# Kernel optimization log

Hardware: AMD Instinct MI355X
Metric: run time of the kernel (lower is better)

Reference implementation:

```python
import jax, jax.numpy as jnp
import numpy as np

WS = 8        # window size
NH = 8        # num heads


def setup_inputs() -> dict:
    key = jax.random.key(0)
    ks = jax.random.split(key, 6)
    B, C, H, W = 8, 256, 64, 64
    Cr = C // 4
    s = lambda n: 1.0 / np.sqrt(n)
    return {
        "x": jax.random.normal(ks[0], (B, C, H, W), jnp.float32),
        "ca_w1": jax.random.normal(ks[1], (Cr, C), jnp.float32) * s(C),
        "ca_b1": jnp.zeros((Cr,), jnp.float32),
        "ca_w2": jax.random.normal(ks[2], (C, Cr), jnp.float32) * s(Cr),
        "ca_b2": jnp.zeros((C,), jnp.float32),
        "in_proj_w": jax.random.normal(ks[3], (3 * C, C), jnp.float32) * s(C),
        "in_proj_b": jnp.zeros((3 * C,), jnp.float32),
        "out_proj_w": jax.random.normal(ks[4], (C, C), jnp.float32) * s(C),
        "out_proj_b": jnp.zeros((C,), jnp.float32),
    }


def reference(x, ca_w1, ca_b1, ca_w2, ca_b2, in_proj_w, in_proj_b, out_proj_w, out_proj_b):
    B, C, H, W = x.shape
    # ---- channel SE gate: AdaptiveAvgPool2d(1) -> 1x1 conv == linear ----
    pooled = x.mean(axis=(2, 3))                                   # [B, C]
    h1 = jax.nn.relu(pooled @ ca_w1.T + ca_b1)                     # [B, C/4]
    ca = jax.nn.sigmoid(h1 @ ca_w2.T + ca_b2)                      # [B, C]
    x = x * ca[:, :, None, None]

    # ---- window partition (non-overlapping unfold) ----
    Hw, Ww = H // WS, W // WS
    nwin = Hw * Ww
    xw = x.reshape(B, C, Hw, WS, Ww, WS).transpose(0, 1, 2, 4, 3, 5)   # [B,C,Hw,Ww,ws,ws]
    # view(B,C,nwin,ws*ws).permute(2,0,3,1).reshape(nwin*B, ws*ws, C)
    xw = xw.reshape(B, C, nwin, WS * WS).transpose(2, 0, 3, 1).reshape(nwin * B, WS * WS, C)

    # ---- nn.MultiheadAttention with batch_first=False: (L, N, E) ----
    # L = nwin*B (sequence!), N = ws*ws (batch!), E = C  -- faithful to source quirk
    L, N, _ = xw.shape
    hd = C // NH
    qkv = xw @ in_proj_w.T + in_proj_b                             # [L, N, 3C]
    q, k, v = jnp.split(qkv, 3, axis=-1)
    to_heads = lambda t: t.reshape(L, N, NH, hd).transpose(1, 2, 0, 3)  # [N, NH, L, hd]
    q, k, v = to_heads(q), to_heads(k), to_heads(v)
    scale = 1.0 / jnp.sqrt(jnp.asarray(hd, x.dtype))
    attn = jax.nn.softmax(jnp.einsum("nhld,nhmd->nhlm", q * scale, k), axis=-1)
    o = jnp.einsum("nhlm,nhmd->nhld", attn, v)                     # [N, NH, L, hd]
    o = o.transpose(2, 0, 1, 3).reshape(L, N, C)
    o = o @ out_proj_w.T + out_proj_b                              # [L, N, C]

    # ---- reshape back; nearest interpolate H*W -> H*W is identity ----
    o = o.reshape(nwin, B, WS * WS, C).transpose(1, 3, 0, 2)       # [B, C, nwin, ws*ws]
    x_out = o.reshape(B, C, H, W)
    return x + x_out
```

## Files before the change

### kernel.cpp

```cpp
#include <hip/hip_runtime.h>
#include <hip/hip_bf16.h>
#include <math.h>


typedef unsigned short ushort_t;
typedef unsigned int uint_t;
typedef __attribute__((ext_vector_type(8))) short bf16x8;
typedef __attribute__((ext_vector_type(4))) float f32x4;

#define ALPHA 0.25503486f

__device__ __forceinline__ uint_t pk_rne(float a, float b) {
    __hip_bfloat16 ha = __float2bfloat16(a), hb = __float2bfloat16(b);
    ushort_t ua = *(ushort_t*)&ha, ub = *(ushort_t*)&hb;
    return (uint_t)ua | ((uint_t)ub << 16);
}

__device__ __forceinline__ uint_t pk2(float a, float b) {
    union { float f; uint_t u; } ua, ub; ua.f = a; ub.f = b;
    return __builtin_amdgcn_perm(ua.u, ub.u, 0x03020706u);
}

__device__ __forceinline__ void gl_lds16(const ushort_t* g, ushort_t* l) {
    __builtin_amdgcn_global_load_lds(
        (__attribute__((address_space(1))) unsigned int*)(g),
        (__attribute__((address_space(3))) unsigned int*)(l), 16, 0, 0);
}

__global__ __launch_bounds__(256) void k_pool(const float* __restrict__ x,
                                              float* __restrict__ pooled) {
    int bc = blockIdx.x;
    const float4* row4 = (const float4*)(x + (size_t)bc * 4096);
    float s = 0.f;
    for (int i = threadIdx.x; i < 1024; i += 256) {
        float4 v = row4[i];
        s += v.x + v.y + v.z + v.w;
    }
    __shared__ float red[256];
    red[threadIdx.x] = s;
    __syncthreads();
    for (int o = 128; o > 0; o >>= 1) {
        if (threadIdx.x < o) red[threadIdx.x] += red[threadIdx.x + o];
        __syncthreads();
    }
    if (threadIdx.x == 0) pooled[bc] = red[0] * (1.f / 4096.f);
}

__global__ __launch_bounds__(256) void k_se(const float* __restrict__ pooled,
                                            const float* __restrict__ w1,
                                            const float* __restrict__ b1,
                                            const float* __restrict__ w2,
                                            const float* __restrict__ b2,
                                            float* __restrict__ ca) {
    __shared__ float sp[2048];
    __shared__ float sh1[512];
    int t = threadIdx.x;
    for (int i = t; i < 2048; i += 256) sp[i] = pooled[i];
    __syncthreads();
    for (int o = t; o < 512; o += 256) {
        int b = o >> 6, m = o & 63;
        float s = b1[m];
        const float* wr = w1 + (size_t)m * 256;
        const float* pr = sp + b * 256;
        for (int c = 0; c < 256; c++) s += pr[c] * wr[c];
        sh1[o] = s > 0.f ? s : 0.f;
    }
    __syncthreads();
    for (int o = t; o < 2048; o += 256) {
        int b = o >> 8, m = o & 255;
        float s = b2[m];
        const float* wr = w2 + (size_t)m * 64;
        const float* hr = sh1 + b * 64;
        for (int c = 0; c < 64; c++) s += hr[c] * wr[c];
        ca[o] = 1.f / (1.f + __expf(-s));
    }
}

__global__ __launch_bounds__(256) void k_cvt(const float* __restrict__ src,
                                             ushort_t* __restrict__ dst, int n8,
                                             int scale_n8, float scale) {
    int i = blockIdx.x * 256 + threadIdx.x;
    if (i >= n8) return;
    float sc = (i < scale_n8) ? scale : 1.f;
    const float4* s = (const float4*)src + (size_t)i * 2;
    float4 a = s[0], b = s[1];
    uint4 u;
    u.x = pk_rne(a.x * sc, a.y * sc); u.y = pk_rne(a.z * sc, a.w * sc);
    u.z = pk_rne(b.x * sc, b.y * sc); u.w = pk_rne(b.z * sc, b.w * sc);
    *(uint4*)(dst + (size_t)i * 8) = u;
}

#define GPAD 524
__global__ __launch_bounds__(256) void k_gate(const float* __restrict__ x,
                                              const float* __restrict__ ca,
                                              ushort_t* __restrict__ Ab) {
    __shared__ __align__(16) ushort_t Ls[32 * GPAD];
    __shared__ float sca[32];
    int bx = blockIdx.x;
    int b = bx >> 6, hw = (bx >> 3) & 7, c0 = (bx & 7) * 32;
    int t = threadIdx.x;
    if (t < 32) sca[t] = ca[b * 256 + c0 + t];
    __syncthreads();
    const float4* xb = (const float4*)(x + ((size_t)(b * 256 + c0) * 64 + hw * 8) * 64);
#pragma unroll
    for (int i = 0; i < 16; i++) {
        int f = i * 256 + t;
        int ch = f >> 7, rem = f & 127, r = rem >> 4, w4 = rem & 15;
        float4 v = xb[(size_t)ch * 1024 + r * 16 + w4];
        float g = sca[ch];
        uint2 u;
        u.x = pk_rne(v.x * g, v.y * g);
        u.y = pk_rne(v.z * g, v.w * g);
        *(uint2*)&Ls[ch * GPAD + r * 64 + w4 * 4] = u;
    }
    __syncthreads();
#pragma unroll
    for (int i = 0; i < 8; i++) {
        int q = i * 256 + t;
        int rr = q >> 2, part = q & 3;
        int ww = rr >> 6, p = rr & 63;
        int px = (p >> 3) * 64 + ww * 8 + (p & 7);
        const ushort_t* ls = &Ls[part * 8 * GPAD + px];
        uint4 u;
        u.x = (uint_t)ls[0]        | ((uint_t)ls[GPAD] << 16);
        u.y = (uint_t)ls[2 * GPAD] | ((uint_t)ls[3 * GPAD] << 16);
        u.z = (uint_t)ls[4 * GPAD] | ((uint_t)ls[5 * GPAD] << 16);
        u.w = (uint_t)ls[6 * GPAD] | ((uint_t)ls[7 * GPAD] << 16);
        size_t m = (size_t)(((hw * 8 + ww) * 8 + b) * 64 + p);
        *(uint4*)(Ab + m * 256 + c0 + part * 8) = u;
    }
}

__global__ __launch_bounds__(256, 2) void k_gemm_qkv2(const ushort_t* __restrict__ A,
                                                      const ushort_t* __restrict__ Bw,
                                                      const float* __restrict__ bias,
                                                      ushort_t* __restrict__ Qb,
                                                      ushort_t* __restrict__ Kb,
                                                      ushort_t* __restrict__ Vb) {
    __shared__ __align__(16) ushort_t As[2][8192];
    __shared__ __align__(16) ushort_t Bs[2][8192];
    int tid = threadIdx.x;
    int lane = tid & 63, wave = tid >> 6;
    int wm = wave >> 1, wn = wave & 1;
    int col = lane & 15, quad = lane >> 4;
    int orig = blockIdx.x;
    int wgid = (orig & 7) * 192 + (orig >> 3);
    int n0 = (wgid % 6) * 128;
    int m0 = (wgid / 6) * 128;
    int cbase = wave * 64 + lane;

    const ushort_t* asrc[4];
    const ushort_t* bsrc[4];
#pragma unroll
    for (int q = 0; q < 4; q++) {
        int c = q * 256 + cbase;
        int row = c >> 3;
        int kp = (c & 7) ^ (row & 7);
        asrc[q] = A + (size_t)(m0 + row) * 256 + kp * 8;
        bsrc[q] = Bw + (size_t)(n0 + row) * 256 + kp * 8;
    }

    f32x4 acc[4][4];
#pragma unroll
    for (int i = 0; i < 4; i++)
#pragma unroll
        for (int j = 0; j < 4; j++) acc[i][j] = (f32x4){0.f, 0.f, 0.f, 0.f};

#pragma unroll
    for (int q = 0; q < 4; q++) {
        gl_lds16(asrc[q], &As[0][(q * 4 + wave) * 512]);
        gl_lds16(bsrc[q], &Bs[0][(q * 4 + wave) * 512]);
    }
    __syncthreads();

#pragma unroll
    for (int t = 0; t < 4; t++) {
        if (t < 3) {
            int k0 = (t + 1) * 64;
            int nb = (t + 1) & 1;
#pragma unroll
            for (int q = 0; q < 4; q++) {
                gl_lds16(asrc[q] + k0, &As[nb][(q * 4 + wave) * 512]);
                gl_lds16(bsrc[q] + k0, &Bs[nb][(q * 4 + wave) * 512]);
            }
        }
        const ushort_t* Ac = As[t & 1];
        const ushort_t* Bc = Bs[t & 1];
#pragma unroll
        for (int kk = 0; kk < 2; kk++) {
            bf16x8 af[4], bfg[4];
#pragma unroll
            for (int i = 0; i < 4; i++) {
                int row = wm * 64 + i * 16 + col;
                af[i] = *(const bf16x8*)&Ac[row * 64 + ((kk * 4 + quad) ^ (row & 7)) * 8];
            }
#pragma unroll
            for (int j = 0; j < 4; j++) {
                int row = wn * 64 + j * 16 + col;
                bfg[j] = *(const bf16x8*)&Bc[row * 64 + ((kk * 4 + quad) ^ (row & 7)) * 8];
            }
#pragma unroll
            for (int i = 0; i < 4; i++)
#pragma unroll
                for (int j = 0; j < 4; j++)
                    acc[i][j] = __builtin_amdgcn_mfma_f32_16x16x32_bf16(bfg[j], af[i], acc[i][j], 0, 0, 0);
        }
        __syncthreads();
    }

    int sec = n0 >> 8;
    ushort_t* dst = (sec == 0) ? Qb : (sec == 1) ? Kb : Vb;
    float bsc = (sec == 0) ? ALPHA : 1.f;
    int nb = (n0 & 255) + wn * 64 + quad * 4;
#pragma unroll
    for (int j = 0; j < 4; j++) {
        float4 bv = *(const float4*)(bias + n0 + wn * 64 + j * 16 + quad * 4);
        bv.x *= bsc; bv.y *= bsc; bv.z *= bsc; bv.w *= bsc;
#pragma unroll
        for (int i = 0; i < 4; i++) {
            int m = m0 + wm * 64 + i * 16 + col;
            uint2 st;
            st.x = pk_rne(acc[i][j][0] + bv.x, acc[i][j][1] + bv.y);
            st.y = pk_rne(acc[i][j][2] + bv.z, acc[i][j][3] + bv.w);
            *(uint2*)(dst + (size_t)m * 256 + nb + j * 16) = st;
        }
    }
}

__global__ __launch_bounds__(512, 4) void k_attn(const ushort_t* __restrict__ Qb,
                                                 const ushort_t* __restrict__ Kb,
                                                 const ushort_t* __restrict__ Vb,
                                                 ushort_t* __restrict__ AO) {
    __shared__ __align__(16) ushort_t Ks[512 * 32];
    __shared__ __align__(16) ushort_t Vt[32 * 512];
    int p = blockIdx.x >> 3, h = blockIdx.x & 7;
    int tid = threadIdx.x;
    int lane = tid & 63, wave = tid >> 6;
    int col = lane & 15, quad = lane >> 4;

#pragma unroll
    for (int it = 0; it < 4; it++) {
        int u = it * 512 + tid;
        int key = u >> 2, oct = u & 3;
        size_t grow = ((size_t)(key * 64 + p)) * 256 + h * 32 + oct * 8;
        int ck = oct ^ ((key >> 3) & 3);
        *(bf16x8*)&Ks[key * 32 + ck * 8] = *(const bf16x8*)(Kb + grow);
    }
#pragma unroll
    for (int it = 0; it < 2; it++) {
        int u = it * 512 + tid;
        int kp = u >> 2, oct = u & 3;
        int k0 = kp * 2;
        size_t g0 = ((size_t)(k0 * 64 + p)) * 256 + h * 32 + oct * 8;
        bf16x8 v0 = *(const bf16x8*)(Vb + g0);
        bf16x8 v1 = *(const bf16x8*)(Vb + g0 + 16384);
        int kc = kp >> 2;
#pragma unroll
        for (int j = 0; j < 8; j++) {
            int vc = oct * 8 + j;
            int kcs = kc ^ (vc & 7) ^ ((vc >> 3) << 1);
            uint_t pkv = (uint_t)(ushort_t)v0[j] | ((uint_t)(ushort_t)v1[j] << 16);
            *(uint_t*)&Vt[vc * 512 + kcs * 8 + (k0 & 7)] = pkv;
        }
    }

    bf16x8 qfrag[4];
#pragma unroll
    for (int i = 0; i < 4; i++) {
        int qt = wave * 4 + i;
        qfrag[i] = *(const bf16x8*)(Qb + ((size_t)((qt * 16 + col) * 64 + p)) * 256 + h * 32 + quad * 8);
    }

    f32x4 O0[4], O1[4];
    float qsum[4];
#pragma unroll
    for (int i = 0; i < 4; i++) {
        O0[i] = (f32x4){0.f, 0.f, 0.f, 0.f};
        O1[i] = (f32x4){0.f, 0.f, 0.f, 0.f};
        qsum[i] = 0.f;
    }
    const f32x4 zero = {0.f, 0.f, 0.f, 0.f};
    int R = col >> 2, r4 = lane & 3;
    int krow0 = 8 * R + r4;
    int vc0 = col, vc1 = col + 16;
    int sw0 = (vc0 & 7) ^ ((vc0 >> 3) << 1);
    int sw1 = (vc1 & 7) ^ ((vc1 >> 3) << 1);

    __syncthreads();

    for (int c = 0; c < 512; c += 32) {
        int row0 = c + krow0;
        int row1 = row0 + 4;
        int ckq = quad ^ ((row0 >> 3) & 3);
        bf16x8 kf0 = *(const bf16x8*)&Ks[row0 * 32 + ckq * 8];
        bf16x8 kf1 = *(const bf16x8*)&Ks[row1 * 32 + ckq * 8];
        int kc = (c >> 3) + quad;
        bf16x8 vf0 = *(const bf16x8*)&Vt[vc0 * 512 + ((kc ^ sw0) * 8)];
        bf16x8 vf1 = *(const bf16x8*)&Vt[vc1 * 512 + ((kc ^ sw1) * 8)];
#pragma unroll
        for (int i = 0; i < 4; i++) {
            f32x4 s0 = __builtin_amdgcn_mfma_f32_16x16x32_bf16(kf0, qfrag[i], zero, 0, 0, 0);
            f32x4 s1 = __builtin_amdgcn_mfma_f32_16x16x32_bf16(kf1, qfrag[i], zero, 0, 0, 0);
            float p0[4], p1[4];
#pragma unroll
            for (int r = 0; r < 4; r++) {
                p0[r] = __builtin_amdgcn_exp2f(s0[r]);
                p1[r] = __builtin_amdgcn_exp2f(s1[r]);
            }
            qsum[i] += ((p0[0] + p0[1]) + (p0[2] + p0[3])) + ((p1[0] + p1[1]) + (p1[2] + p1[3]));
            union { uint_t u[4]; bf16x8 v; } pb;
            pb.u[0] = pk2(p0[0], p0[1]);
            pb.u[1] = pk2(p0[2], p0[3]);
            pb.u[2] = pk2(p1[0], p1[1]);
            pb.u[3] = pk2(p1[2], p1[3]);
            O0[i] = __builtin_amdgcn_mfma_f32_16x16x32_bf16(vf0, pb.v, O0[i], 0, 0, 0);
            O1[i] = __builtin_amdgcn_mfma_f32_16x16x32_bf16(vf1, pb.v, O1[i], 0, 0, 0);
        }
    }

#pragma unroll
    for (int i = 0; i < 4; i++) {
        float s = qsum[i];
        s += __shfl_xor(s, 16);
        s += __shfl_xor(s, 32);
        float inv = 1.f / s;
        int qt = wave * 4 + i;
        ushort_t* dst = AO + ((size_t)((qt * 16 + col) * 64 + p)) * 256 + h * 32;
        uint2 st0, st1;
        st0.x = pk_rne(O0[i][0] * inv, O0[i][1] * inv);
        st0.y = pk_rne(O0[i][2] * inv, O0[i][3] * inv);
        st1.x = pk_rne(O1[i][0] * inv, O1[i][1] * inv);
        st1.y = pk_rne(O1[i][2] * inv, O1[i][3] * inv);
        *(uint2*)(dst + quad * 4) = st0;
        *(uint2*)(dst + 16 + quad * 4) = st1;
    }
}

__global__ __launch_bounds__(256, 2) void k_gemm_out2(const ushort_t* __restrict__ A,
                                                      const ushort_t* __restrict__ Bw,
                                                      const float* __restrict__ bias,
                                                      const float* __restrict__ x,
                                                      const float* __restrict__ ca,
                                                      float* __restrict__ out) {
    __shared__ __align__(16) ushort_t As[2][8192];
    __shared__ __align__(16) ushort_t Bs[2][8192];
    int tid = threadIdx.x;
    int lane = tid & 63, wave = tid >> 6;
    int wm = wave >> 1, wn = wave & 1;
    int col = lane & 15, quad = lane >> 4;
    int orig = blockIdx.x;
    int wgid = (orig & 7) * 64 + (orig >> 3);
    int n0 = (wgid & 1) * 128;
    int m0 = (wgid >> 1) * 128;
    int cbase = wave * 64 + lane;

    const ushort_t* asrc[4];
    const ushort_t* bsrc[4];
#pragma unroll
    for (int q = 0; q < 4; q++) {
        int c = q * 256 + cbase;
        int row = c >> 3;
        int kp = (c & 7) ^ (row & 7);
        asrc[q] = A + (size_t)(m0 + row) * 256 + kp * 8;
        bsrc[q] = Bw + (size_t)(n0 + row) * 256 + kp * 8;
    }

    f32x4 acc[4][4];
#pragma unroll
    for (int i = 0; i < 4; i++)
#pragma unroll
        for (int j = 0; j < 4; j++) acc[i][j] = (f32x4){0.f, 0.f, 0.f, 0.f};

#pragma unroll
    for (int q = 0; q < 4; q++) {
        gl_lds16(asrc[q], &As[0][(q * 4 + wave) * 512]);
        gl_lds16(bsrc[q], &Bs[0][(q * 4 + wave) * 512]);
    }
    __syncthreads();

#pragma unroll
    for (int t = 0; t < 4; t++) {
        if (t < 3) {
            int k0 = (t + 1) * 64;
            int nb = (t + 1) & 1;
#pragma unroll
            for (int q = 0; q < 4; q++) {
                gl_lds16(asrc[q] + k0, &As[nb][(q * 4 + wave) * 512]);
                gl_lds16(bsrc[q] + k0, &Bs[nb][(q * 4 + wave) * 512]);
            }
        }
        const ushort_t* Ac = As[t & 1];
        const ushort_t* Bc = Bs[t & 1];
#pragma unroll
        for (int kk = 0; kk < 2; kk++) {
            bf16x8 af[4], bfg[4];
#pragma unroll
            for (int i = 0; i < 4; i++) {
                int row = wm * 64 + i * 16 + col;
                af[i] = *(const bf16x8*)&Ac[row * 64 + ((kk * 4 + quad) ^ (row & 7)) * 8];
            }
#pragma unroll
            for (int j = 0; j < 4; j++) {
                int row = wn * 64 + j * 16 + col;
                bfg[j] = *(const bf16x8*)&Bc[row * 64 + ((kk * 4 + quad) ^ (row & 7)) * 8];
            }
#pragma unroll
            for (int i = 0; i < 4; i++)
#pragma unroll
                for (int j = 0; j < 4; j++)
                    acc[i][j] = __builtin_amdgcn_mfma_f32_16x16x32_bf16(bfg[j], af[i], acc[i][j], 0, 0, 0);
        }
        __syncthreads();
    }

    int lw = (m0 + wm * 64) >> 6;
    int b = lw & 7, w_idx = lw >> 3;
#pragma unroll
    for (int j = 0; j < 4; j++) {
        int nbase = n0 + wn * 64 + j * 16 + quad * 4;
        float4 bv = *(const float4*)(bias + nbase);
        float4 cv = *(const float4*)(ca + b * 256 + nbase);
#pragma unroll
        for (int i = 0; i < 4; i++) {
            int p = i * 16 + col;
#pragma unroll
            for (int r = 0; r < 4; r++) {
                int n = nbase + r;
                float bias_r = (r == 0) ? bv.x : (r == 1) ? bv.y : (r == 2) ? bv.z : bv.w;
                float ca_r = (r == 0) ? cv.x : (r == 1) ? cv.y : (r == 2) ? cv.z : cv.w;
                size_t oi = (((size_t)b * 256 + n) * 64 + w_idx) * 64 + p;
                out[oi] = acc[i][j][r] + bias_r + x[oi] * ca_r;
            }
        }
    }
}

extern "C" void kernel_launch(void* const* d_in, const int* in_sizes, int n_in,
                              void* d_out, int out_size, void* d_ws, size_t ws_size,
                              hipStream_t stream) {
    const float* x     = (const float*)d_in[0];
    const float* ca_w1 = (const float*)d_in[1];
    const float* ca_b1 = (const float*)d_in[2];
    const float* ca_w2 = (const float*)d_in[3];
    const float* ca_b2 = (const float*)d_in[4];
    const float* ipw   = (const float*)d_in[5];
    const float* ipb   = (const float*)d_in[6];
    const float* opw   = (const float*)d_in[7];
    const float* opb   = (const float*)d_in[8];
    float* out = (float*)d_out;

    char* ws = (char*)d_ws;
    const size_t MB16 = 16777216ull;
    ushort_t* Qb = (ushort_t*)(ws + 0);
    ushort_t* Kb = (ushort_t*)(ws + MB16);
    ushort_t* Vb = (ushort_t*)(ws + 2 * MB16);
    float* pooled = (float*)(ws + 3 * MB16);
    float* ca     = (float*)(ws + 3 * MB16 + 8192);

    ushort_t* Ab  = (ushort_t*)d_out;
    ushort_t* Wqb = (ushort_t*)((char*)d_out + MB16);
    ushort_t* Wob = Vb;

    k_cvt<<<96, 256, 0, stream>>>(ipw, Wqb, 24576, 8192, ALPHA);
    k_pool<<<2048, 256, 0, stream>>>(x, pooled);
    k_se<<<1, 256, 0, stream>>>(pooled, ca_w1, ca_b1, ca_w2, ca_b2, ca);
    k_gate<<<512, 256, 0, stream>>>(x, ca, Ab);
    k_gemm_qkv2<<<1536, 256, 0, stream>>>(Ab, Wqb, ipb, Qb, Kb, Vb);
    k_attn<<<512, 512, 0, stream>>>(Qb, Kb, Vb, Qb );
    k_cvt<<<32, 256, 0, stream>>>(opw, Wob, 8192, 0, 1.f);
    k_gemm_out2<<<512, 256, 0, stream>>>(Qb, Wob, opb, x, ca, out);
}
```

Measured before the change: 208.5 us.

## Fuse pooling with weight conversion and widen QKV GEMM tile to 128x256

Pooling and both weight bf16 conversions now run in one launch. When the workspace is large enough, the out-proj conversion moves early into a dedicated workspace slot, removing one later launch. The QKV GEMM now computes a 128x256 tile (a full Q, K or V section) per block with half the blocks, which raises B-tile reuse. It drops LDS double buffering for a single buffer loaded each k-step, so load latency may no longer be hidden, and it uses more accumulator registers.

```diff
diff --git a/kernel.cpp b/kernel.cpp
--- a/kernel.cpp
+++ b/kernel.cpp
@@ -27,52 +27,46 @@
         (__attribute__((address_space(3))) unsigned int*)(l), 16, 0, 0);
 }
 
-__global__ __launch_bounds__(256) void k_pool(const float* __restrict__ x,
-                                              float* __restrict__ pooled) {
-    int bc = blockIdx.x;
-    const float4* row4 = (const float4*)(x + (size_t)bc * 4096);
-    float s = 0.f;
-    for (int i = threadIdx.x; i < 1024; i += 256) {
-        float4 v = row4[i];
-        s += v.x + v.y + v.z + v.w;
-    }
-    __shared__ float red[256];
-    red[threadIdx.x] = s;
-    __syncthreads();
-    for (int o = 128; o > 0; o >>= 1) {
-        if (threadIdx.x < o) red[threadIdx.x] += red[threadIdx.x + o];
+__global__ __launch_bounds__(256) void k_pre(const float* __restrict__ x,
+                                             float* __restrict__ pooled,
+                                             const float* __restrict__ ipw,
+                                             ushort_t* __restrict__ Wqb,
+                                             const float* __restrict__ opw,
+                                             ushort_t* __restrict__ Wob) {
+    int bx = blockIdx.x;
+    int t = threadIdx.x;
+    if (bx < 2048) {
+        const float4* row4 = (const float4*)(x + (size_t)bx * 4096);
+        float s = 0.f;
+        for (int i = t; i < 1024; i += 256) {
+            float4 v = row4[i];
+            s += v.x + v.y + v.z + v.w;
+        }
+        __shared__ float red[256];
+        red[t] = s;
         __syncthreads();
-    }
-    if (threadIdx.x == 0) pooled[bc] = red[0] * (1.f / 4096.f);
-}
-
-__global__ __launch_bounds__(256) void k_se(const float* __restrict__ pooled,
-                                            const float* __restrict__ w1,
-                                            const float* __restrict__ b1,
-                                            const float* __restrict__ w2,
-                                            const float* __restrict__ b2,
-                                            float* __restrict__ ca) {
-    __shared__ float sp[2048];
-    __shared__ float sh1[512];
-    int t = threadIdx.x;
-    for (int i = t; i < 2048; i += 256) sp[i] = pooled[i];
-    __syncthreads();
-    for (int o = t; o < 512; o += 256) {
-        int b = o >> 6, m = o & 63;
-        float s = b1[m];
-        const float* wr = w1 + (size_t)m * 256;
-        const float* pr = sp + b * 256;
-        for (int c = 0; c < 256; c++) s += pr[c] * wr[c];
-        sh1[o] = s > 0.f ? s : 0.f;
-    }
-    __syncthreads();
-    for (int o = t; o < 2048; o += 256) {
-        int b = o >> 8, m = o & 255;
-        float s = b2[m];
-        const float* wr = w2 + (size_t)m * 64;
-        const float* hr = sh1 + b * 64;
-        for (int c = 0; c < 64; c++) s += hr[c] * wr[c];
-        ca[o] = 1.f / (1.f + __expf(-s));
+        for (int o = 128; o > 0; o >>= 1) {
+            if (t < o) red[t] += red[t + o];
+            __syncthreads();
+        }
+        if (t == 0) pooled[bx] = red[0] * (1.f / 4096.f);
+    } else if (bx < 2144) {
+        int i = (bx - 2048) * 256 + t;
+        float sc = (i < 8192) ? ALPHA : 1.f;
+        const float4* s4 = (const float4*)ipw + (size_t)i * 2;
+        float4 a = s4[0], b = s4[1];
+        uint4 u;
+        u.x = pk_rne(a.x * sc, a.y * sc); u.y = pk_rne(a.z * sc, a.w * sc);
+        u.z = pk_rne(b.x * sc, b.y * sc); u.w = pk_rne(b.z * sc, b.w * sc);
+        *(uint4*)(Wqb + (size_t)i * 8) = u;
+    } else {
+        int i = (bx - 2144) * 256 + t;
+        const float4* s4 = (const float4*)opw + (size_t)i * 2;
+        float4 a = s4[0], b = s4[1];
+        uint4 u;
+        u.x = pk_rne(a.x, a.y); u.y = pk_rne(a.z, a.w);
+        u.z = pk_rne(b.x, b.y); u.w = pk_rne(b.z, b.w);
+        *(uint4*)(Wob + (size_t)i * 8) = u;
     }
 }
 
@@ -88,6 +82,36 @@
     u.x = pk_rne(a.x * sc, a.y * sc); u.y = pk_rne(a.z * sc, a.w * sc);
     u.z = pk_rne(b.x * sc, b.y * sc); u.w = pk_rne(b.z * sc, b.w * sc);
     *(uint4*)(dst + (size_t)i * 8) = u;
+}
+
+__global__ __launch_bounds__(256) void k_se(const float* __restrict__ pooled,
+                                            const float* __restrict__ w1,
+                                            const float* __restrict__ b1,
+                                            const float* __restrict__ w2,
+                                            const float* __restrict__ b2,
+                                            float* __restrict__ ca) {
+    __shared__ float sp[2048];
+    __shared__ float sh1[512];
+    int t = threadIdx.x;
+    for (int i = t; i < 2048; i += 256) sp[i] = pooled[i];
+    __syncthreads();
+    for (int o = t; o < 512; o += 256) {
+        int b = o >> 6, m = o & 63;
+        float s = b1[m];
+        const float* wr = w1 + (size_t)m * 256;
+        const float* pr = sp + b * 256;
+        for (int c = 0; c < 256; c++) s += pr[c] * wr[c];
+        sh1[o] = s > 0.f ? s : 0.f;
+    }
+    __syncthreads();
+    for (int o = t; o < 2048; o += 256) {
+        int b = o >> 8, m = o & 255;
+        float s = b2[m];
+        const float* wr = w2 + (size_t)m * 64;
+        const float* hr = sh1 + b * 64;
+        for (int c = 0; c < 64; c++) s += hr[c] * wr[c];
+        ca[o] = 1.f / (1.f + __expf(-s));
+    }
 }
 
 #define GPAD 524
@@ -131,90 +155,85 @@
     }
 }
 
-__global__ __launch_bounds__(256, 2) void k_gemm_qkv2(const ushort_t* __restrict__ A,
+__global__ __launch_bounds__(256, 2) void k_gemm_qkv3(const ushort_t* __restrict__ A,
                                                       const ushort_t* __restrict__ Bw,
                                                       const float* __restrict__ bias,
                                                       ushort_t* __restrict__ Qb,
                                                       ushort_t* __restrict__ Kb,
                                                       ushort_t* __restrict__ Vb) {
-    __shared__ __align__(16) ushort_t As[2][8192];
-    __shared__ __align__(16) ushort_t Bs[2][8192];
+    __shared__ __align__(16) ushort_t As[8192];
+    __shared__ __align__(16) ushort_t Bs[16384];
     int tid = threadIdx.x;
     int lane = tid & 63, wave = tid >> 6;
     int wm = wave >> 1, wn = wave & 1;
     int col = lane & 15, quad = lane >> 4;
     int orig = blockIdx.x;
-    int wgid = (orig & 7) * 192 + (orig >> 3);
-    int n0 = (wgid % 6) * 128;
-    int m0 = (wgid / 6) * 128;
+    int xcd = orig & 7;
+    int i96 = orig >> 3;
+    int mi = i96 / 3;
+    int sec = i96 - mi * 3;
+    int m0 = (xcd * 32 + mi) * 128;
+    const ushort_t* Bsec = Bw + ((size_t)sec << 16);
+
     int cbase = wave * 64 + lane;
-
     const ushort_t* asrc[4];
-    const ushort_t* bsrc[4];
+    const ushort_t* bsrc[8];
 #pragma unroll
     for (int q = 0; q < 4; q++) {
         int c = q * 256 + cbase;
         int row = c >> 3;
         int kp = (c & 7) ^ (row & 7);
         asrc[q] = A + (size_t)(m0 + row) * 256 + kp * 8;
-        bsrc[q] = Bw + (size_t)(n0 + row) * 256 + kp * 8;
-    }
-
-    f32x4 acc[4][4];
+    }
+#pragma unroll
+    for (int q = 0; q < 8; q++) {
+        int c = q * 256 + cbase;
+        int row = c >> 3;
+        int kp = (c & 7) ^ (row & 7);
+        bsrc[q] = Bsec + (size_t)row * 256 + kp * 8;
+    }
+
+    f32x4 acc[4][8];
 #pragma unroll
     for (int i = 0; i < 4; i++)
 #pragma unroll
-        for (int j = 0; j < 4; j++) acc[i][j] = (f32x4){0.f, 0.f, 0.f, 0.f};
-
-#pragma unroll
-    for (int q = 0; q < 4; q++) {
-        gl_lds16(asrc[q], &As[0][(q * 4 + wave) * 512]);
-        gl_lds16(bsrc[q], &Bs[0][(q * 4 + wave) * 512]);
-    }
-    __syncthreads();
-
-#pragma unroll
+        for (int j = 0; j < 8; j++) acc[i][j] = (f32x4){0.f, 0.f, 0.f, 0.f};
+
     for (int t = 0; t < 4; t++) {
-        if (t < 3) {
-            int k0 = (t + 1) * 64;
-            int nb = (t + 1) & 1;
-#pragma unroll
-            for (int q = 0; q < 4; q++) {
-                gl_lds16(asrc[q] + k0, &As[nb][(q * 4 + wave) * 512]);
-                gl_lds16(bsrc[q] + k0, &Bs[nb][(q * 4 + wave) * 512]);
-            }
-        }
-        const ushort_t* Ac = As[t & 1];
-        const ushort_t* Bc = Bs[t & 1];
+        int k0 = t * 64;
+#pragma unroll
+        for (int q = 0; q < 4; q++) gl_lds16(asrc[q] + k0, &As[(q * 4 + wave) * 512]);
+#pragma unroll
+        for (int q = 0; q < 8; q++) gl_lds16(bsrc[q] + k0, &Bs[(q * 4 + wave) * 512]);
+        __syncthreads();
 #pragma unroll
         for (int kk = 0; kk < 2; kk++) {
-            bf16x8 af[4], bfg[4];
+            bf16x8 af[4], bfg[8];
 #pragma unroll
             for (int i = 0; i < 4; i++) {
                 int row = wm * 64 + i * 16 + col;
-                af[i] = *(const bf16x8*)&Ac[row * 64 + ((kk * 4 + quad) ^ (row & 7)) * 8];
-            }
-#pragma unroll
-            for (int j = 0; j < 4; j++) {
-                int row = wn * 64 + j * 16 + col;
-                bfg[j] = *(const bf16x8*)&Bc[row * 64 + ((kk * 4 + quad) ^ (row & 7)) * 8];
+                af[i] = *(const bf16x8*)&As[row * 64 + ((kk * 4 + quad) ^ (row & 7)) * 8];
+            }
+#pragma unroll
+            for (int j = 0; j < 8; j++) {
+                int row = wn * 128 + j * 16 + col;
+                bfg[j] = *(const bf16x8*)&Bs[row * 64 + ((kk * 4 + quad) ^ (row & 7)) * 8];
             }
 #pragma unroll
             for (int i = 0; i < 4; i++)
 #pragma unroll
-                for (int j = 0; j < 4; j++)
+                for (int j = 0; j < 8; j++)
                     acc[i][j] = __builtin_amdgcn_mfma_f32_16x16x32_bf16(bfg[j], af[i], acc[i][j], 0, 0, 0);
         }
         __syncthreads();
     }
 
-    int sec = n0 >> 8;
     ushort_t* dst = (sec == 0) ? Qb : (sec == 1) ? Kb : Vb;
     float bsc = (sec == 0) ? ALPHA : 1.f;
-    int nb = (n0 & 255) + wn * 64 + quad * 4;
-#pragma unroll
-    for (int j = 0; j < 4; j++) {
-        float4 bv = *(const float4*)(bias + n0 + wn * 64 + j * 16 + quad * 4);
+    int nb0 = wn * 128 + quad * 4;
+#pragma unroll
+    for (int j = 0; j < 8; j++) {
+        float4 bv = *(const float4*)(bias + sec * 256 + nb0 + j * 16);
         bv.x *= bsc; bv.y *= bsc; bv.z *= bsc; bv.w *= bsc;
 #pragma unroll
         for (int i = 0; i < 4; i++) {
@@ -222,7 +241,7 @@
             uint2 st;
             st.x = pk_rne(acc[i][j][0] + bv.x, acc[i][j][1] + bv.y);
             st.y = pk_rne(acc[i][j][2] + bv.z, acc[i][j][3] + bv.w);
-            *(uint2*)(dst + (size_t)m * 256 + nb + j * 16) = st;
+            *(uint2*)(dst + (size_t)m * 256 + nb0 + j * 16) = st;
         }
     }
 }
@@ -459,14 +478,16 @@
 
     ushort_t* Ab  = (ushort_t*)d_out;
     ushort_t* Wqb = (ushort_t*)((char*)d_out + MB16);
-    ushort_t* Wob = Vb;
-
-    k_cvt<<<96, 256, 0, stream>>>(ipw, Wqb, 24576, 8192, ALPHA);
-    k_pool<<<2048, 256, 0, stream>>>(x, pooled);
+
+    const size_t WOB_OFF = 3 * MB16 + 16384;
+    bool wob_early = (ws_size >= WOB_OFF + 131072);
+    ushort_t* Wob = wob_early ? (ushort_t*)(ws + WOB_OFF) : Vb;
+
+    k_pre<<<wob_early ? 2176 : 2144, 256, 0, stream>>>(x, pooled, ipw, Wqb, opw, Wob);
     k_se<<<1, 256, 0, stream>>>(pooled, ca_w1, ca_b1, ca_w2, ca_b2, ca);
     k_gate<<<512, 256, 0, stream>>>(x, ca, Ab);
-    k_gemm_qkv2<<<1536, 256, 0, stream>>>(Ab, Wqb, ipb, Qb, Kb, Vb);
+    k_gemm_qkv3<<<768, 256, 0, stream>>>(Ab, Wqb, ipb, Qb, Kb, Vb);
     k_attn<<<512, 512, 0, stream>>>(Qb, Kb, Vb, Qb );
-    k_cvt<<<32, 256, 0, stream>>>(opw, Wob, 8192, 0, 1.f);
+    if (!wob_early) k_cvt<<<32, 256, 0, stream>>>(opw, Vb, 8192, 0, 1.f);
     k_gemm_out2<<<512, 256, 0, stream>>>(Qb, Wob, opb, x, ca, out);
 }
```

New measurement: 200.6 us. 1.04x faster.
